# Kernel optimization log

Measured on AMD Instinct MI355X. Metric: run time of the kernel, lower is better.

## Reference

```python
import jax, jax.numpy as jnp
import numpy as np
from jax import lax

RADIUS = (5, 5, 5)
EPS = 1e-5


def _box_sum(x, radius=RADIUS):
    # Separable all-ones box filter == F.conv3d(x, ones((1,1,)+radius), padding='same')
    # x: [N, 1, D, H, W]
    dn = lax.conv_dimension_numbers(x.shape, (1, 1) + radius, ('NCDHW', 'OIDHW', 'NCDHW'))
    for axis, k in zip((2, 3, 4), radius):
        kshape = [1, 1, 1, 1, 1]
        kshape[axis] = k
        kern = jnp.ones(kshape, dtype=x.dtype)
        dn_ax = lax.conv_dimension_numbers(x.shape, tuple(kshape), ('NCDHW', 'OIDHW', 'NCDHW'))
        x = lax.conv_general_dilated(x, kern, window_strides=(1, 1, 1), padding='SAME',
                                     dimension_numbers=dn_ax)
    return x


def _image_gradient(img):
    # torch.gradient over spatial dims (central diff interior, one-sided edges)
    g = jnp.gradient(img, axis=(2, 3, 4))
    return jnp.concatenate(g, axis=1)  # [N, 3, D, H, W]


def setup_inputs() -> dict:
    key = jax.random.key(0)
    k1, k2, k3, k4 = jax.random.split(key, 4)
    shape = (1, 1, 192, 192, 192)
    moving_image = jax.random.normal(k1, shape, dtype=jnp.float32)
    fixed_image = jax.random.normal(k2, shape, dtype=jnp.float32)
    moving_mask = jax.random.randint(k3, shape, 0, 2).astype(jnp.bool_)
    fixed_mask = jax.random.randint(k4, shape, 0, 2).astype(jnp.bool_)
    original_image_spacing = jnp.ones((3,), dtype=jnp.int32)
    return {
        'moving_image': moving_image,
        'fixed_image': fixed_image,
        'moving_mask': moving_mask,
        'fixed_mask': fixed_mask,
        'original_image_spacing': original_image_spacing,
    }


def reference(moving_image, fixed_image, moving_mask, fixed_mask, original_image_spacing):
    npix = float(np.prod(RADIUS))  # 125

    # dual method: union mask applied to both gradients, total grad halved
    union = jnp.logical_or(moving_mask, fixed_mask).astype(moving_image.dtype)
    grad_moving = _image_gradient(moving_image) * union
    grad_fixed = _image_gradient(fixed_image) * union
    total_grad = (grad_moving + grad_fixed) * 0.5

    sum_m = _box_sum(moving_image)
    sum_f = _box_sum(fixed_image)
    sum_mm = _box_sum(moving_image * moving_image)
    sum_ff = _box_sum(fixed_image * fixed_image)
    sum_mf = _box_sum(moving_image * fixed_image)

    moving_mean = sum_m / npix
    fixed_mean = sum_f / npix

    var_m = sum_mm - 2 * moving_mean * sum_m + npix * moving_mean * moving_mean
    var_f = sum_ff - 2 * fixed_mean * sum_f + npix * fixed_mean * fixed_mean
    var_mf = var_m * var_f
    cross = sum_mf - fixed_mean * sum_m - moving_mean * sum_f + npix * moving_mean * fixed_mean

    moving_mean_centered = moving_image - moving_mean
    fixed_mean_centered = fixed_image - fixed_mean

    mask = (var_mf > EPS) & (var_f > EPS) & (fixed_mean_centered != 0.0) & (moving_mean_centered != 0.0)
    var_mf_safe = jnp.where(mask, var_mf, 1.0)
    var_f_safe = jnp.where(mask, var_f, 1.0)
    factor = jnp.where(
        mask,
        2.0 * cross / var_mf_safe * (moving_mean_centered - cross * fixed_mean_centered / var_f_safe),
        0.0,
    )

    return -1.0 * factor * total_grad
```

## Files before the change

### kernel.cpp

```cpp
#include <hip/hip_runtime.h>


#define DD 192
#define HH 192
#define WW 192
#define NVOX (DD * HH * WW)
#define SLICE (HH * WW)
#define TS 16
#define RR 20
#define RW 24
#define ZSEG 12
#define NBX 12
#define NBY 12
#define NBZ 16
#define NBLK (NBX * NBY * NBZ)
#define PER_XCD (NBLK / 8)

__global__ __launch_bounds__(256)
void ncc_forces_kernel(const float* __restrict__ mimg,
                       const float* __restrict__ fimg,
                       const int*   __restrict__ mmask,
                       const int*   __restrict__ fmask,
                       float* __restrict__ out)
{
    __shared__ float rawm[2][RR][RW];
    __shared__ float rawf[2][RR][RW];
    __shared__ float xs[5][RR][20];
    __shared__ float Tf[4][RR][20];
    __shared__ float box[2][TS][5][20];

    const int b  = blockIdx.x;
    const int L  = (b & 7) * PER_XCD + (b >> 3);
    const int bz = L / (NBX * NBY);
    const int r_ = L - bz * (NBX * NBY);
    const int by = r_ / NBX;
    const int bx = r_ - by * NBX;

    const int tid = threadIdx.x;
    const int tx = tid & 15, ty = tid >> 4;
    const int x0 = bx * TS, y0 = by * TS, z0 = bz * ZSEG;

    const int  simg   = tid / 120;
    const bool stager = (simg < 2);
    const int  st     = tid - simg * 120;
    const int  srow   = st / 6;
    const int  squad  = st - srow * 6;
    const int  sgy    = y0 - 2 + srow;
    const int  sgx    = x0 - 4 + 4 * squad;
    const bool sin_   = (sgy >= 0) && (sgy < HH) && (sgx >= 0) && (sgx <= WW - 4);
    const float* sptr = (simg == 1) ? fimg : mimg;
    float* sldsb = (simg == 1) ? &rawf[0][0][0] : &rawm[0][0][0];
    const int  sloff  = srow * RW + 4 * squad;

    float4 pref = make_float4(0, 0, 0, 0);
    auto prefetch = [&](int zz) {
        pref = make_float4(0, 0, 0, 0);
        if (stager && sin_ && zz >= 0 && zz < DD)
            pref = *(const float4*)(sptr + ((size_t)zz * HH + sgy) * WW + sgx);
    };

    float ring[5][5];
#pragma unroll
    for (int s = 0; s < 5; ++s)
#pragma unroll
        for (int f = 0; f < 5; ++f) ring[s][f] = 0.f;
    float cm[5] = {0, 0, 0, 0, 0}, cf[5] = {0, 0, 0, 0, 0};

    const int gx = x0 + tx, gy = y0 + ty;
    const int vbase = (z0 * HH + gy) * WW + gx;
    int umN = 0, ufN = 0;

    prefetch(z0 - 2);

    for (int n = 0; n <= ZSEG + 4; ++n) {
        const int zc = z0 - 2 + n;
        const int sw = n & 1;
        const int z  = zc - 3;
        const bool emitv = (n >= 5);

        if (stager) *(float4*)(sldsb + sw * (RR * RW) + sloff) = pref;
        prefetch(zc + 1);

        const int um = umN, uf = ufN;
        if (n >= 4 && n < ZSEG + 4) {
            const int vn = vbase + (n - 4) * SLICE;
            umN = __builtin_nontemporal_load(mmask + vn);
            ufN = __builtin_nontemporal_load(fmask + vn);
        }

        __syncthreads();

        if (tid < 80) {
            const int yy = tid >> 2;
            const int t4 = (tid & 3) * 4;
            const float4 A0 = *(const float4*)&rawm[sw][yy][t4];
            const float4 A1 = *(const float4*)&rawm[sw][yy][t4 + 4];
            const float2 A2 = *(const float2*)&rawm[sw][yy][t4 + 8];
            const float4 B0 = *(const float4*)&rawf[sw][yy][t4];
            const float4 B1 = *(const float4*)&rawf[sw][yy][t4 + 4];
            const float2 B2 = *(const float2*)&rawf[sw][yy][t4 + 8];
            const float a[10]  = {A0.x, A0.y, A0.z, A0.w, A1.x, A1.y, A1.z, A1.w, A2.x, A2.y};
            const float bb[10] = {B0.x, B0.y, B0.z, B0.w, B1.x, B1.y, B1.z, B1.w, B2.x, B2.y};
            float p[10], s, w0, w1, w2, w3;
#pragma unroll
            for (int f = 0; f < 5; ++f) {
#pragma unroll
                for (int i = 2; i < 10; ++i) {
                    p[i] = (f == 0) ? a[i] : (f == 1) ? bb[i] :
                           (f == 2) ? a[i] * a[i] : (f == 3) ? bb[i] * bb[i] : a[i] * bb[i];
                }
                s = p[2] + p[3] + p[4] + p[5] + p[6]; w0 = s;
                s += p[7] - p[2]; w1 = s;
                s += p[8] - p[3]; w2 = s;
                s += p[9] - p[4]; w3 = s;
                *(float4*)&xs[f][yy][t4] = make_float4(w0, w1, w2, w3);
            }
            const int tw = n & 3;
            *(float4*)&Tf[tw][yy][t4] =
                make_float4(a[2] + bb[2], a[3] + bb[3], a[4] + bb[4], a[5] + bb[5]);
            if (t4 == 12)
                *(float4*)&Tf[tw][yy][16] =
                    make_float4(a[6] + bb[6], a[7] + bb[7], a[8] + bb[8], a[9] + bb[9]);
        }

        {
            const float ncm = rawm[sw][ty + 2][tx + 4];
            const float ncf = rawf[sw][ty + 2][tx + 4];
#pragma unroll
            for (int s2 = 4; s2 > 0; --s2) { cm[s2] = cm[s2 - 1]; cf[s2] = cf[s2 - 1]; }
            cm[0] = ncm; cf[0] = ncf;
        }
        if (n >= 1) {
            const int pp = (n - 1) & 1;
            const float* bq = &box[pp][tx][0][ty];
            const float s0 = bq[0], s1 = bq[20], s2v = bq[40], s3 = bq[60], s4 = bq[80];
#pragma unroll
            for (int s = 0; s < 4; ++s)
#pragma unroll
                for (int f = 0; f < 5; ++f) ring[s][f] = ring[s + 1][f];
            ring[4][0] = s0; ring[4][1] = s1; ring[4][2] = s2v; ring[4][3] = s3; ring[4][4] = s4;
        }

        if (emitv) {
            float sum_m = 0.f, sum_f = 0.f, sum_mm = 0.f, sum_ff = 0.f, sum_mf = 0.f;
#pragma unroll
            for (int s = 0; s < 5; ++s) {
                sum_m  += ring[s][0];
                sum_f  += ring[s][1];
                sum_mm += ring[s][2];
                sum_ff += ring[s][3];
                sum_mf += ring[s][4];
            }
            const int vidx = vbase + (n - 5) * SLICE;
            const int tsl = (n + 1) & 3;
            const int cy = ty + 2;
            const float mc = cm[3];
            const float fc = cf[3];
            const float Tc = mc + fc;

            const float* tp = &Tf[tsl][cy][tx + 1];
            const float Txm = tp[0], Txp = tp[2];
            const float* tq = &Tf[tsl][cy - 1][tx + 2];
            const float Tym = tq[0], Typ = tq[40];

            float gsx, gsy, gsz;
            if (gx == 0)          gsx = Txp - Tc;
            else if (gx == WW-1)  gsx = Tc - Txm;
            else                  gsx = 0.5f * (Txp - Txm);
            if (gy == 0)          gsy = Typ - Tc;
            else if (gy == HH-1)  gsy = Tc - Tym;
            else                  gsy = 0.5f * (Typ - Tym);
            const float Tzm = cm[4] + cf[4], Tzp = cm[2] + cf[2];
            if (z == 0)           gsz = Tzp - Tc;
            else if (z == DD-1)   gsz = Tc - Tzm;
            else                  gsz = 0.5f * (Tzp - Tzm);

            const float u = ((um != 0) || (uf != 0)) ? 1.0f : 0.0f;

            const float npix = 125.0f;
            const float inv_npix = 1.0f / 125.0f;
            const float mean_m = sum_m * inv_npix;
            const float mean_f = sum_f * inv_npix;
            const float var_m = sum_mm - 2.0f * mean_m * sum_m + npix * mean_m * mean_m;
            const float var_f = sum_ff - 2.0f * mean_f * sum_f + npix * mean_f * mean_f;
            const float var_mf = var_m * var_f;
            const float cross = sum_mf - mean_f * sum_m - mean_m * sum_f + npix * mean_m * mean_f;
            const float mmc = mc - mean_m;
            const float fmc = fc - mean_f;
            const bool ok = (var_mf > 1e-5f) && (var_f > 1e-5f) && (fmc != 0.0f) && (mmc != 0.0f);
            float factor = 0.0f;
            if (ok) factor = 2.0f * cross / var_mf * (mmc - cross * fmc / var_f);

            const float nf = -factor * 0.5f * u;
            out[vidx]            = nf * gsz;
            out[NVOX + vidx]     = nf * gsy;
            out[2 * NVOX + vidx] = nf * gsx;
        }

        __syncthreads();

        if (tid < 160) {
            const int x  = tid & 15;
            const int c8 = ((tid >> 4) & 1) * 8;
            const int f  = tid >> 5;
            const float* xp = &xs[f][c8][x];
            float v[12];
#pragma unroll
            for (int j = 0; j < 12; ++j) v[j] = xp[20 * j];
            float o[8];
            float s = v[0] + v[1] + v[2] + v[3] + v[4];
            o[0] = s;
#pragma unroll
            for (int j = 1; j < 8; ++j) { s += v[j + 4] - v[j - 1]; o[j] = s; }
            float* bp = &box[n & 1][x][f][c8];
            *(float4*)bp       = make_float4(o[0], o[1], o[2], o[3]);
            *(float4*)(bp + 4) = make_float4(o[4], o[5], o[6], o[7]);
        }
    }
}

extern "C" void kernel_launch(void* const* d_in, const int* in_sizes, int n_in,
                              void* d_out, int out_size, void* d_ws, size_t ws_size,
                              hipStream_t stream)
{
    const float* mimg  = (const float*)d_in[0];
    const float* fimg  = (const float*)d_in[1];
    const int*   mmask = (const int*)d_in[2];
    const int*   fmask = (const int*)d_in[3];
    float* out = (float*)d_out;

    dim3 grid(NBLK, 1, 1);
    dim3 block(256, 1, 1);
    hipLaunchKernelGGL(ncc_forces_kernel, grid, block, 0, stream,
                       mimg, fimg, mmask, fmask, out);
}
```

Measured before the change: 211.2 us.

## Software-pipeline box-filter stages to use one barrier per z-slice

Restructures the per-slice loop so the x-pass, y-pass and output stages work on different z-slices in the same iteration, with double-buffered xs and a five-deep Tf ring. This removes one __syncthreads per iteration and lets the y-pass threads (96-255) run concurrently with the x-pass threads (0-79). The cost is one extra pipeline iteration, more shared memory, and a deeper register history for the centre values.

New measurement: 216.4 us. 1.02x slower.

```diff
diff --git a/kernel.cpp b/kernel.cpp
--- a/kernel.cpp
+++ b/kernel.cpp
@@ -25,8 +25,8 @@
 {
     __shared__ float rawm[2][RR][RW];
     __shared__ float rawf[2][RR][RW];
-    __shared__ float xs[5][RR][20];
-    __shared__ float Tf[4][RR][20];
+    __shared__ float xs[2][5][RR][16];
+    __shared__ float Tf[5][18][20];
     __shared__ float box[2][TS][5][20];
 
     const int b  = blockIdx.x;
@@ -64,33 +64,31 @@
     for (int s = 0; s < 5; ++s)
 #pragma unroll
         for (int f = 0; f < 5; ++f) ring[s][f] = 0.f;
-    float cm[5] = {0, 0, 0, 0, 0}, cf[5] = {0, 0, 0, 0, 0};
+    float cm[6] = {0, 0, 0, 0, 0, 0}, cf[6] = {0, 0, 0, 0, 0, 0};
 
     const int gx = x0 + tx, gy = y0 + ty;
     const int vbase = (z0 * HH + gy) * WW + gx;
     int umN = 0, ufN = 0;
 
     prefetch(z0 - 2);
-
-    for (int n = 0; n <= ZSEG + 4; ++n) {
-        const int zc = z0 - 2 + n;
-        const int sw = n & 1;
-        const int z  = zc - 3;
-        const bool emitv = (n >= 5);
-
-        if (stager) *(float4*)(sldsb + sw * (RR * RW) + sloff) = pref;
-        prefetch(zc + 1);
-
+    if (stager) *(float4*)(sldsb + 0 * (RR * RW) + sloff) = pref;
+    prefetch(z0 - 1);
+
+    for (int k = 0; k <= ZSEG + 5; ++k) {
+        __syncthreads();
+
+        const int sw = k & 1;
         const int um = umN, uf = ufN;
-        if (n >= 4 && n < ZSEG + 4) {
-            const int vn = vbase + (n - 4) * SLICE;
+        if (k >= 5 && k <= ZSEG + 4) {
+            const int vn = vbase + (k - 5) * SLICE;
             umN = __builtin_nontemporal_load(mmask + vn);
             ufN = __builtin_nontemporal_load(fmask + vn);
         }
 
-        __syncthreads();
-
-        if (tid < 80) {
+        if (stager) *(float4*)(sldsb + ((k + 1) & 1) * (RR * RW) + sloff) = pref;
+        prefetch(z0 + k);
+
+        if (tid < 80 && k <= ZSEG + 3) {
             const int yy = tid >> 2;
             const int t4 = (tid & 3) * 4;
             const float4 A0 = *(const float4*)&rawm[sw][yy][t4];
@@ -113,26 +111,47 @@
                 s += p[7] - p[2]; w1 = s;
                 s += p[8] - p[3]; w2 = s;
                 s += p[9] - p[4]; w3 = s;
-                *(float4*)&xs[f][yy][t4] = make_float4(w0, w1, w2, w3);
+                *(float4*)&xs[sw][f][yy][t4] = make_float4(w0, w1, w2, w3);
             }
-            const int tw = n & 3;
-            *(float4*)&Tf[tw][yy][t4] =
-                make_float4(a[2] + bb[2], a[3] + bb[3], a[4] + bb[4], a[5] + bb[5]);
-            if (t4 == 12)
-                *(float4*)&Tf[tw][yy][16] =
-                    make_float4(a[6] + bb[6], a[7] + bb[7], a[8] + bb[8], a[9] + bb[9]);
+            if (yy >= 1 && yy <= 18) {
+                const int tw = k % 5;
+                *(float4*)&Tf[tw][yy - 1][t4] =
+                    make_float4(a[2] + bb[2], a[3] + bb[3], a[4] + bb[4], a[5] + bb[5]);
+                if (t4 == 12)
+                    *(float4*)&Tf[tw][yy - 1][16] =
+                        make_float4(a[6] + bb[6], a[7] + bb[7], a[8] + bb[8], a[9] + bb[9]);
+            }
         }
 
         {
             const float ncm = rawm[sw][ty + 2][tx + 4];
             const float ncf = rawf[sw][ty + 2][tx + 4];
 #pragma unroll
-            for (int s2 = 4; s2 > 0; --s2) { cm[s2] = cm[s2 - 1]; cf[s2] = cf[s2 - 1]; }
+            for (int s2 = 5; s2 > 0; --s2) { cm[s2] = cm[s2 - 1]; cf[s2] = cf[s2 - 1]; }
             cm[0] = ncm; cf[0] = ncf;
         }
-        if (n >= 1) {
-            const int pp = (n - 1) & 1;
-            const float* bq = &box[pp][tx][0][ty];
+
+        if (tid >= 96 && k >= 1 && k <= ZSEG + 4) {
+            const int ytid = tid - 96;
+            const int x  = ytid & 15;
+            const int c8 = ((ytid >> 4) & 1) * 8;
+            const int f  = ytid >> 5;
+            const float* xp = &xs[(k - 1) & 1][f][c8][x];
+            float v[12];
+#pragma unroll
+            for (int j = 0; j < 12; ++j) v[j] = xp[16 * j];
+            float o[8];
+            float s = v[0] + v[1] + v[2] + v[3] + v[4];
+            o[0] = s;
+#pragma unroll
+            for (int j = 1; j < 8; ++j) { s += v[j + 4] - v[j - 1]; o[j] = s; }
+            float* bp = &box[k & 1][x][f][c8];
+            *(float4*)bp       = make_float4(o[0], o[1], o[2], o[3]);
+            *(float4*)(bp + 4) = make_float4(o[4], o[5], o[6], o[7]);
+        }
+
+        if (k >= 2) {
+            const float* bq = &box[(k - 1) & 1][tx][0][ty];
             const float s0 = bq[0], s1 = bq[20], s2v = bq[40], s3 = bq[60], s4 = bq[80];
 #pragma unroll
             for (int s = 0; s < 4; ++s)
@@ -141,7 +160,7 @@
             ring[4][0] = s0; ring[4][1] = s1; ring[4][2] = s2v; ring[4][3] = s3; ring[4][4] = s4;
         }
 
-        if (emitv) {
+        if (k >= 6) {
             float sum_m = 0.f, sum_f = 0.f, sum_mm = 0.f, sum_ff = 0.f, sum_mf = 0.f;
 #pragma unroll
             for (int s = 0; s < 5; ++s) {
@@ -151,16 +170,16 @@
                 sum_ff += ring[s][3];
                 sum_mf += ring[s][4];
             }
-            const int vidx = vbase + (n - 5) * SLICE;
-            const int tsl = (n + 1) & 3;
-            const int cy = ty + 2;
-            const float mc = cm[3];
-            const float fc = cf[3];
+            const int z    = z0 - 6 + k;
+            const int vidx = vbase + (k - 6) * SLICE;
+            const int tsl  = (k + 1) % 5;
+            const float mc = cm[4];
+            const float fc = cf[4];
             const float Tc = mc + fc;
 
-            const float* tp = &Tf[tsl][cy][tx + 1];
+            const float* tp = &Tf[tsl][ty + 1][tx + 1];
             const float Txm = tp[0], Txp = tp[2];
-            const float* tq = &Tf[tsl][cy - 1][tx + 2];
+            const float* tq = &Tf[tsl][ty][tx + 2];
             const float Tym = tq[0], Typ = tq[40];
 
             float gsx, gsy, gsz;
@@ -170,7 +189,7 @@
             if (gy == 0)          gsy = Typ - Tc;
             else if (gy == HH-1)  gsy = Tc - Tym;
             else                  gsy = 0.5f * (Typ - Tym);
-            const float Tzm = cm[4] + cf[4], Tzp = cm[2] + cf[2];
+            const float Tzm = cm[5] + cf[5], Tzp = cm[3] + cf[3];
             if (z == 0)           gsz = Tzp - Tc;
             else if (z == DD-1)   gsz = Tc - Tzm;
             else                  gsz = 0.5f * (Tzp - Tzm);
@@ -196,26 +215,6 @@
             out[NVOX + vidx]     = nf * gsy;
             out[2 * NVOX + vidx] = nf * gsx;
         }
-
-        __syncthreads();
-
-        if (tid < 160) {
-            const int x  = tid & 15;
-            const int c8 = ((tid >> 4) & 1) * 8;
-            const int f  = tid >> 5;
-            const float* xp = &xs[f][c8][x];
-            float v[12];
-#pragma unroll
-            for (int j = 0; j < 12; ++j) v[j] = xp[20 * j];
-            float o[8];
-            float s = v[0] + v[1] + v[2] + v[3] + v[4];
-            o[0] = s;
-#pragma unroll
-            for (int j = 1; j < 8; ++j) { s += v[j + 4] - v[j - 1]; o[j] = s; }
-            float* bp = &box[n & 1][x][f][c8];
-            *(float4*)bp       = make_float4(o[0], o[1], o[2], o[3]);
-            *(float4*)(bp + 4) = make_float4(o[4], o[5], o[6], o[7]);
-        }
     }
 }
 
```
